# Kernel tuning notes

Measured on AMD Instinct MI355X. Metric: run time of the kernel, lower is better.

The kernel has to match this reference:

```python
import jax, jax.numpy as jnp
import numpy as np

B, N, DV = 32, 1024, 512
L, S, DT = 256, 8, 512
VOCAB = 1024
BAND = 16
LN_EPS = 1e-5


def setup_inputs() -> dict:
    key = jax.random.key(0)
    ks = jax.random.split(key, 12)
    w = lambda k, shp: jax.random.normal(k, shp, dtype=jnp.float32) * 0.02
    return {
        "vis_tokens": jax.random.normal(ks[0], (B, N, DV), dtype=jnp.float32),
        "txt_ctx_ids": jax.random.randint(ks[1], (B, L, S), 0, VOCAB, dtype=jnp.int32),
        "emb_w": w(ks[2], (VOCAB, DT)),        # embedding table, tied with classifier
        "wq": w(ks[3], (DV, DT)),              # q_proj: d_txt -> d_vis
        "wk": w(ks[4], (DV, DV)),
        "wv": w(ks[5], (DV, DV)),
        "wv2t": w(ks[6], (DT, DV)),            # vis2txt: d_vis -> d_txt
        "dw_k": w(ks[7], (DT, 1, 3)),          # depthwise conv1d kernel (O, I/g=1, K)
        "pw_k": w(ks[8], (DT, DT, 1)),         # pointwise conv1d kernel
        "ln_g": jnp.ones((DT,), jnp.float32),
        "ln_b": jnp.zeros((DT,), jnp.float32),
        "dir_alpha": jnp.float32(0.2),
    }


def reference(vis_tokens, txt_ctx_ids, emb_w, wq, wk, wv, wv2t, dw_k, pw_k, ln_g, ln_b, dir_alpha):
    b, n, dv = vis_tokens.shape
    E = emb_w[txt_ctx_ids]                       # [B, L, S, Dt]
    bl = b * E.shape[1]
    x = E.reshape(bl, E.shape[2], DT).transpose(0, 2, 1)  # [B*L, Dt, S]
    dn = ('NCH', 'OIH', 'NCH')
    h = jax.lax.conv_general_dilated(x, dw_k, (1,), 'SAME', dimension_numbers=dn,
                                     feature_group_count=DT)
    y = jax.lax.conv_general_dilated(jax.nn.silu(h), pw_k, (1,), 'SAME', dimension_numbers=dn)
    x = x + y
    m = x.mean(axis=2)                           # [B*L, Dt]
    mu = m.mean(-1, keepdims=True)
    var = ((m - mu) ** 2).mean(-1, keepdims=True)
    q_txt = ((m - mu) * jax.lax.rsqrt(var + LN_EPS) * ln_g + ln_b).reshape(b, -1, DT)  # [B, L, Dt]

    Q = q_txt @ wq.T                             # [B, L, Dv]
    K = vis_tokens @ wk.T                        # [B, N, Dv]
    V = vis_tokens @ wv.T
    logits = jnp.einsum('bld,bnd->bln', Q, K) * (dv ** -0.5)

    # linear centers (torch linspace(0, N-1, L).long() truncates toward zero)
    centers = jnp.linspace(0.0, n - 1, q_txt.shape[1]).astype(jnp.int32)  # [L]
    centers = jnp.broadcast_to(centers[None, :], (b, q_txt.shape[1]))
    idx = jnp.arange(n)[None, None, :]
    signed = (centers[..., None] - idx).astype(jnp.float32)
    logits = logits + dir_alpha * (signed / (BAND + 1e-6))
    keep = jnp.abs(idx - centers[..., None]) <= BAND
    logits = jnp.where(keep, logits, -jnp.inf)

    A = jax.nn.softmax(logits, axis=-1)          # [B, L, N]
    Fv = jnp.einsum('bln,bnd->bld', A, V)        # dropout in source is undefined attr; identity
    H = Fv @ wv2t.T                              # [B, L, Dt]
    cls = H @ emb_w.T                            # tied classifier
    return (cls, H, A)
```

## Files before the change

### kernel.cpp

```cpp
#include <hip/hip_runtime.h>
#include <cmath>

typedef unsigned short u16;
typedef __attribute__((ext_vector_type(8))) short bf16x8;
typedef __attribute__((ext_vector_type(4))) float f32x4;
typedef __attribute__((ext_vector_type(8))) unsigned short u16x8;

#define B_  32
#define N_  1024
#define L_  256
#define S_  8
#define DT_ 512
#define BAND_ 16

__device__ __forceinline__ u16 f2bf(float f) {
  union { float f; unsigned u; } x; x.f = f;
  unsigned r = (x.u + 0x7fffu + ((x.u >> 16) & 1u)) >> 16;
  return (u16)r;
}
__device__ __forceinline__ float bf2f(u16 h) {
  union { unsigned u; float f; } x; x.u = ((unsigned)h) << 16;
  return x.f;
}
__device__ __forceinline__ unsigned cvtpk(float lo, float hi) {
  unsigned r;
  asm volatile("v_cvt_pk_bf16_f32 %0, %1, %2" : "=v"(r) : "v"(lo), "v"(hi));
  return r;
}

#define B1_WAIT(N)                                       \
  asm volatile("s_waitcnt vmcnt(" #N ")" ::: "memory");  \
  __builtin_amdgcn_s_barrier();                          \
  __builtin_amdgcn_sched_barrier(0);
#define B2_BAR()                                         \
  __builtin_amdgcn_sched_barrier(0);                     \
  __builtin_amdgcn_s_barrier();

__global__ __launch_bounds__(256) void mega_front(
    const float* __restrict__ vis, u16* __restrict__ visb,
    const float* __restrict__ e, const float* __restrict__ q,
    const float* __restrict__ k, const float* __restrict__ v,
    const float* __restrict__ t, const float* __restrict__ pw,
    u16* __restrict__ eo, u16* __restrict__ qo, u16* __restrict__ kvo,
    u16* __restrict__ to, u16* __restrict__ po,
    const int* __restrict__ ids, const float* __restrict__ dwk,
    u16* __restrict__ shm, float* __restrict__ mbuf) {
  const int blk = blockIdx.x;
  const int tid = threadIdx.x;
  if (blk < 4096) {
    const int c0 = tid * 2;
#pragma unroll
    for (int ii = 0; ii < 2; ++ii) {
      const int bl = blk * 2 + ii;
      int sid[S_];
#pragma unroll
      for (int s = 0; s < S_; ++s) sid[s] = ids[bl * S_ + s];
      float2 x2[S_];
#pragma unroll
      for (int s = 0; s < S_; ++s)
        x2[s] = *(const float2*)(e + (size_t)sid[s] * DT_ + c0);
      const float2 d01 = *(const float2*)(dwk + 3 * c0 + 0);
      const float2 d23 = *(const float2*)(dwk + 3 * c0 + 2);
      const float2 d45 = *(const float2*)(dwk + 3 * c0 + 4);
      float me0 = 0.f, sh0 = 0.f, me1 = 0.f, sh1 = 0.f;
#pragma unroll
      for (int s = 0; s < S_; ++s) {
        const float xm0 = (s > 0) ? x2[s - 1].x : 0.0f;
        const float xp0 = (s < S_ - 1) ? x2[s + 1].x : 0.0f;
        const float xm1 = (s > 0) ? x2[s - 1].y : 0.0f;
        const float xp1 = (s < S_ - 1) ? x2[s + 1].y : 0.0f;
        const float h0 = d01.x * xm0 + d01.y * x2[s].x + d23.x * xp0;
        const float h1 = d23.y * xm1 + d45.x * x2[s].y + d45.y * xp1;
        sh0 += h0 / (1.0f + __expf(-h0));
        sh1 += h1 / (1.0f + __expf(-h1));
        me0 += x2[s].x;
        me1 += x2[s].y;
      }
      ((unsigned*)shm)[((size_t)bl * DT_ + c0) >> 1] =
          cvtpk(sh0 * (1.0f / S_), sh1 * (1.0f / S_));
      *(float2*)(mbuf + (size_t)bl * DT_ + c0) =
          make_float2(me0 * (1.0f / S_), me1 * (1.0f / S_));
    }
  } else {
    for (int ch = blk - 4096; ch < 18176; ch += 8192) {
      if (ch < 16384) {
        int i = ch * 256 + tid;
        float4 vv = ((const float4*)vis)[i];
        uint2 o;
        o.x = cvtpk(vv.x, vv.y);
        o.y = cvtpk(vv.z, vv.w);
        ((uint2*)visb)[i] = o;
      } else {
        int i = (ch - 16384) * 256 + tid;
        const float* src; u16* dst; int soff, doff;
        if (i < 131072)      { src = e;  dst = eo;  soff = i;          doff = soff; }
        else if (i < 196608) { src = q;  dst = qo;  soff = i - 131072; doff = soff; }
        else if (i < 262144) { src = k;  dst = kvo; soff = i - 196608; doff = soff; }
        else if (i < 327680) { src = v;  dst = kvo; soff = i - 262144; doff = soff + 65536; }
        else if (i < 393216) { src = t;  dst = to;  soff = i - 327680; doff = soff; }
        else                 { src = pw; dst = po;  soff = i - 393216; doff = soff; }
        float4 vv = ((const float4*)src)[soff];
        uint2 o;
        o.x = cvtpk(vv.x, vv.y);
        o.y = cvtpk(vv.z, vv.w);
        ((uint2*)dst)[doff] = o;
      }
    }
  }
}

__global__ __launch_bounds__(512) void gemm_kv_v2(
    const u16* __restrict__ A, const u16* __restrict__ B,
    u16* __restrict__ Cb, int M, int N, int K) {
  __shared__ u16 As[16384];
  __shared__ u16 Bs[8192];
  const int tid = threadIdx.x;
  const int w = tid >> 6;
  const int lane = tid & 63;
  const int wm = w >> 1, wn = w & 1;

  const int gx = gridDim.x;
  const int bid = blockIdx.y * gx + blockIdx.x;
  const int nwg = gx * gridDim.y;
  const int logical = (bid & 7) * (nwg >> 3) + (bid >> 3);
  const int bm = (logical / gx) << 8;
  const int bn = (logical % gx) << 7;

  const int rowA0 = (w << 5) + (lane >> 2);
  const int rowA1 = rowA0 + 16;
  const int rowB = (w << 4) + (lane >> 2);
  const int gac = (((lane & 3) ^ ((lane >> 3) & 3)) << 3);
  const u16* AgS0 = A + (size_t)(bm + rowA0) * K + gac;
  const u16* AgS1 = A + (size_t)(bm + rowA1) * K + gac;
  const u16* BgS = B + (size_t)(bn + rowB) * K + gac;
  const int ldsA0 = (w << 10);
  const int ldsA1 = (w << 10) + 512;
  const int ldsB = (w << 9);

#define STAGE(step)                                                           \
  {                                                                           \
    const int bufA_ = ((step) & 1) << 13;                                     \
    const int bufB_ = ((step) & 1) << 12;                                     \
    const int ks_ = (step) << 5;                                              \
    __builtin_amdgcn_global_load_lds(                                         \
        (const __attribute__((address_space(1))) void*)(AgS0 + ks_),          \
        (__attribute__((address_space(3))) void*)(As + bufA_ + ldsA0), 16, 0, 0); \
    __builtin_amdgcn_global_load_lds(                                         \
        (const __attribute__((address_space(1))) void*)(AgS1 + ks_),          \
        (__attribute__((address_space(3))) void*)(As + bufA_ + ldsA1), 16, 0, 0); \
    __builtin_amdgcn_global_load_lds(                                         \
        (const __attribute__((address_space(1))) void*)(BgS + ks_),           \
        (__attribute__((address_space(3))) void*)(Bs + bufB_ + ldsB), 16, 0, 0); \
  }

  const int kg = lane >> 4;
  int aoff[4], boff[4];
#pragma unroll
  for (int m = 0; m < 4; ++m) {
    const int r = (wm << 6) + (m << 4) + (lane & 15);
    aoff[m] = (r << 5) + ((kg ^ ((r >> 1) & 3)) << 3);
  }
#pragma unroll
  for (int n = 0; n < 4; ++n) {
    const int r = (wn << 6) + (n << 4) + (lane & 15);
    boff[n] = (r << 5) + ((kg ^ ((r >> 1) & 3)) << 3);
  }

  f32x4 acc[4][4];
#pragma unroll
  for (int m = 0; m < 4; ++m)
#pragma unroll
    for (int n = 0; n < 4; ++n) acc[m][n] = (f32x4){0.f, 0.f, 0.f, 0.f};

#define GROUP_BODY(sbuf)                                                      \
  {                                                                           \
    const u16* Ab = As + ((sbuf) << 13);                                      \
    const u16* Bb = Bs + ((sbuf) << 12);                                      \
    bf16x8 af[4], bfr[4];                                                     \
    _Pragma("unroll")                                                         \
    for (int m = 0; m < 4; ++m) af[m] = *(const bf16x8*)(Ab + aoff[m]);       \
    _Pragma("unroll")                                                         \
    for (int n = 0; n < 4; ++n) bfr[n] = *(const bf16x8*)(Bb + boff[n]);      \
    asm volatile("s_waitcnt lgkmcnt(0)" ::: "memory");                        \
    __builtin_amdgcn_sched_barrier(0);                                        \
    __builtin_amdgcn_s_setprio(1);                                            \
    _Pragma("unroll")                                                         \
    for (int m = 0; m < 4; ++m)                                               \
      _Pragma("unroll")                                                       \
      for (int n = 0; n < 4; ++n)                                             \
        acc[m][n] = __builtin_amdgcn_mfma_f32_16x16x32_bf16(                  \
            af[m], bfr[n], acc[m][n], 0, 0, 0);                               \
    __builtin_amdgcn_s_setprio(0);                                            \
  }

  const int nt = K >> 5;
  STAGE(0)
  for (int s = 0; s < nt; ++s) {
    __builtin_amdgcn_s_barrier();
    if (s + 1 < nt) {
      STAGE(s + 1)
      B1_WAIT(3)
    } else {
      B1_WAIT(0)
    }
    GROUP_BODY(s & 1)
  }
#undef GROUP_BODY
#undef STAGE

  const int rb = bm + (wm << 6) + ((lane >> 4) << 2);
  const int cb = bn + (wn << 6) + (lane & 15);
#pragma unroll
  for (int m = 0; m < 4; ++m)
#pragma unroll
    for (int n = 0; n < 4; ++n) {
      const int col = cb + (n << 4);
#pragma unroll
      for (int j = 0; j < 4; ++j) {
        size_t idx = (size_t)(rb + (m << 4) + j) * N + col;
        Cb[idx] = f2bf(acc[m][n][j]);
      }
    }
}

template <bool ACC, bool WF32, bool WBF16>
__global__ __launch_bounds__(256) void gemm_mfma(
    const u16* __restrict__ A, const u16* __restrict__ B,
    float* __restrict__ C, u16* __restrict__ Cb, int M, int N, int K) {
  __shared__ u16 As[8192];
  __shared__ u16 Bs[8192];
  const int tid = threadIdx.x;
  const int w = tid >> 6;
  const int lane = tid & 63;

  const int gx = gridDim.x;
  const int bid = blockIdx.y * gx + blockIdx.x;
  const int nwg = gx * gridDim.y;
  const int logical = (bid & 7) * (nwg >> 3) + (bid >> 3);
  const int bm = (logical / gx) << 7;
  const int bn = (logical % gx) << 7;
  const int wr = w >> 1, wc = w & 1;

  const int r0 = (w << 4) + (lane >> 2);
  const int kc = (lane & 3) << 3;
  const u16* Ag0 = A + (size_t)(bm + r0) * K + kc;
  const u16* Ag1 = Ag0 + (size_t)64 * K;
  const u16* Bg0 = B + (size_t)(bn + r0) * K + kc;
  const u16* Bg1 = Bg0 + (size_t)64 * K;

  int aoff[4], boff[4];
#pragma unroll
  for (int m = 0; m < 4; ++m)
    aoff[m] = (((wr << 6) + (m << 4) + (lane & 15)) << 5) + ((lane >> 4) << 3);
#pragma unroll
  for (int n = 0; n < 4; ++n)
    boff[n] = (((wc << 6) + (n << 4) + (lane & 15)) << 5) + ((lane >> 4) << 3);

  f32x4 acc[4][4];
#pragma unroll
  for (int m = 0; m < 4; ++m)
#pragma unroll
    for (int n = 0; n < 4; ++n) acc[m][n] = (f32x4){0.f, 0.f, 0.f, 0.f};

#define STAGE(buf, kt)                                                        \
  {                                                                           \
    u16* as_ = As + (buf) * 4096 + (w << 9);                                  \
    u16* bs_ = Bs + (buf) * 4096 + (w << 9);                                  \
    __builtin_amdgcn_global_load_lds(                                         \
        (const __attribute__((address_space(1))) void*)(Ag0 + (kt)),          \
        (__attribute__((address_space(3))) void*)as_, 16, 0, 0);              \
    __builtin_amdgcn_global_load_lds(                                         \
        (const __attribute__((address_space(1))) void*)(Ag1 + (kt)),          \
        (__attribute__((address_space(3))) void*)(as_ + 2048), 16, 0, 0);     \
    __builtin_amdgcn_global_load_lds(                                         \
        (const __attribute__((address_space(1))) void*)(Bg0 + (kt)),          \
        (__attribute__((address_space(3))) void*)bs_, 16, 0, 0);              \
    __builtin_amdgcn_global_load_lds(                                         \
        (const __attribute__((address_space(1))) void*)(Bg1 + (kt)),          \
        (__attribute__((address_space(3))) void*)(bs_ + 2048), 16, 0, 0);     \
  }

  const int nt = K >> 5;
  STAGE(0, 0);
  int cur = 0;
  for (int t = 0; t < nt; ++t) {
    if (t + 1 < nt) {
      STAGE(cur ^ 1, (t + 1) << 5);
      B1_WAIT(4)
    } else {
      B1_WAIT(0)
    }
    const u16* Ab = As + cur * 4096;
    const u16* Bb = Bs + cur * 4096;
    bf16x8 af[4], bfr[4];
#pragma unroll
    for (int m = 0; m < 4; ++m) af[m] = *(const bf16x8*)(Ab + aoff[m]);
#pragma unroll
    for (int n = 0; n < 4; ++n) bfr[n] = *(const bf16x8*)(Bb + boff[n]);
#pragma unroll
    for (int m = 0; m < 4; ++m)
#pragma unroll
      for (int n = 0; n < 4; ++n)
        acc[m][n] = __builtin_amdgcn_mfma_f32_16x16x32_bf16(
            af[m], bfr[n], acc[m][n], 0, 0, 0);
    B2_BAR()
    cur ^= 1;
  }
#undef STAGE

  const int rb = bm + (wr << 6) + ((lane >> 4) << 2);
  const int cb = bn + (wc << 6) + (lane & 15);
#pragma unroll
  for (int m = 0; m < 4; ++m)
#pragma unroll
    for (int n = 0; n < 4; ++n) {
      int col = cb + (n << 4);
#pragma unroll
      for (int j = 0; j < 4; ++j) {
        size_t idx = (size_t)(rb + (m << 4) + j) * N + col;
        float v = acc[m][n][j];
        if (ACC) v += C[idx];
        if (WF32) C[idx] = v;
        if (WBF16) Cb[idx] = f2bf(v);
      }
    }
}

template <bool ACC, bool WF32, bool WBF16>
__global__ __launch_bounds__(256) void gemm_n64(
    const u16* __restrict__ A, const u16* __restrict__ B,
    float* __restrict__ C, u16* __restrict__ Cb, int M, int N, int K) {
  __shared__ u16 As[8192];
  __shared__ u16 Bs[4096];
  const int tid = threadIdx.x;
  const int w = tid >> 6;
  const int lane = tid & 63;

  const int gx = gridDim.x;
  const int bid = blockIdx.y * gx + blockIdx.x;
  const int nwg = gx * gridDim.y;
  const int logical = (bid & 7) * (nwg >> 3) + (bid >> 3);
  const int bm = (logical / gx) << 7;
  const int bn = (logical % gx) << 6;

  const int r0 = (w << 4) + (lane >> 2);
  const int kc = (lane & 3) << 3;
  const u16* Ag0 = A + (size_t)(bm + r0) * K + kc;
  const u16* Ag1 = Ag0 + (size_t)64 * K;
  const u16* Bg0 = B + (size_t)(bn + r0) * K + kc;

  int aoff[2], boff[4];
#pragma unroll
  for (int m = 0; m < 2; ++m)
    aoff[m] = (((w << 5) + (m << 4) + (lane & 15)) << 5) + ((lane >> 4) << 3);
#pragma unroll
  for (int n = 0; n < 4; ++n)
    boff[n] = (((n << 4) + (lane & 15)) << 5) + ((lane >> 4) << 3);

  f32x4 acc[2][4];
#pragma unroll
  for (int m = 0; m < 2; ++m)
#pragma unroll
    for (int n = 0; n < 4; ++n) acc[m][n] = (f32x4){0.f, 0.f, 0.f, 0.f};

#define STAGE(buf, kt)                                                        \
  {                                                                           \
    u16* as_ = As + (buf) * 4096 + (w << 9);                                  \
    u16* bs_ = Bs + (buf) * 2048 + (w << 9);                                  \
    __builtin_amdgcn_global_load_lds(                                         \
        (const __attribute__((address_space(1))) void*)(Ag0 + (kt)),          \
        (__attribute__((address_space(3))) void*)as_, 16, 0, 0);              \
    __builtin_amdgcn_global_load_lds(                                         \
        (const __attribute__((address_space(1))) void*)(Ag1 + (kt)),          \
        (__attribute__((address_space(3))) void*)(as_ + 2048), 16, 0, 0);     \
    __builtin_amdgcn_global_load_lds(                                         \
        (const __attribute__((address_space(1))) void*)(Bg0 + (kt)),          \
        (__attribute__((address_space(3))) void*)bs_, 16, 0, 0);              \
  }

  const int nt = K >> 5;
  STAGE(0, 0);
  int cur = 0;
  for (int t = 0; t < nt; ++t) {
    if (t + 1 < nt) {
      STAGE(cur ^ 1, (t + 1) << 5);
      B1_WAIT(3)
    } else {
      B1_WAIT(0)
    }
    const u16* Ab = As + cur * 4096;
    const u16* Bb = Bs + cur * 2048;
    bf16x8 af[2], bfr[4];
#pragma unroll
    for (int m = 0; m < 2; ++m) af[m] = *(const bf16x8*)(Ab + aoff[m]);
#pragma unroll
    for (int n = 0; n < 4; ++n) bfr[n] = *(const bf16x8*)(Bb + boff[n]);
#pragma unroll
    for (int m = 0; m < 2; ++m)
#pragma unroll
      for (int n = 0; n < 4; ++n)
        acc[m][n] = __builtin_amdgcn_mfma_f32_16x16x32_bf16(
            af[m], bfr[n], acc[m][n], 0, 0, 0);
    B2_BAR()
    cur ^= 1;
  }
#undef STAGE

  const int rb = bm + (w << 5) + ((lane >> 4) << 2);
  const int cb = bn + (lane & 15);
#pragma unroll
  for (int m = 0; m < 2; ++m)
#pragma unroll
    for (int n = 0; n < 4; ++n) {
      int col = cb + (n << 4);
#pragma unroll
      for (int j = 0; j < 4; ++j) {
        size_t idx = (size_t)(rb + (m << 4) + j) * N + col;
        float v = acc[m][n][j];
        if (ACC) v += C[idx];
        if (WF32) C[idx] = v;
        if (WBF16) Cb[idx] = f2bf(v);
      }
    }
}

__global__ __launch_bounds__(256) void ln_kernel(
    const float* __restrict__ m, const float* __restrict__ g,
    const float* __restrict__ bta, u16* __restrict__ q) {
  int row = blockIdx.x;
  int tid = threadIdx.x;
  float v0 = m[(size_t)row * 512 + tid];
  float v1 = m[(size_t)row * 512 + 256 + tid];
  __shared__ float red[4], red2[4];
  float s = v0 + v1;
#pragma unroll
  for (int d = 32; d; d >>= 1) s += __shfl_xor(s, d);
  if ((tid & 63) == 0) red[tid >> 6] = s;
  __syncthreads();
  float mu = (red[0] + red[1] + red[2] + red[3]) * (1.0f / 512.0f);
  float d0 = v0 - mu, d1 = v1 - mu;
  float s2 = d0 * d0 + d1 * d1;
#pragma unroll
  for (int d = 32; d; d >>= 1) s2 += __shfl_xor(s2, d);
  if ((tid & 63) == 0) red2[tid >> 6] = s2;
  __syncthreads();
  float var = (red2[0] + red2[1] + red2[2] + red2[3]) * (1.0f / 512.0f);
  float r = rsqrtf(var + 1e-5f);
  q[(size_t)row * 512 + tid] = f2bf(d0 * r * g[tid] + bta[tid]);
  q[(size_t)row * 512 + 256 + tid] = f2bf(d1 * r * g[tid + 256] + bta[tid + 256]);
}

__global__ __launch_bounds__(512) void attn_kernel(
    const u16* __restrict__ Qb, const u16* __restrict__ KV,
    const float* __restrict__ alpha_p, float* __restrict__ A,
    u16* __restrict__ Fv) {
  __shared__ u16 KV_s[96 * 512];
  __shared__ u16 Q_s[16 * 520];
  __shared__ float S_s[16 * 100];

  const int bid = blockIdx.x;
  const int logical = (bid & 7) * 64 + (bid >> 3);
  const int b = logical >> 4, lg = logical & 15;
  const int l0 = lg * 16;
  const int tid = threadIdx.x;
  const int w = tid >> 6, lane = tid & 63;
  const float al = *alpha_p;

  const int c_min = (1023 * l0) / 255;
  const int kb0 = min(max(c_min - BAND_, 0), N_ - 96);

  {
    const size_t rowb = (size_t)(b * N_ + kb0);
    for (int rr = 0; rr < 12; ++rr) {
      const int r = w * 12 + rr;
      const u16* src = KV + (rowb + r) * 1024 + ((lane * 8) ^ ((r & 7) << 3));
      u16* dst = KV_s + r * 512;
      __builtin_amdgcn_global_load_lds(
          (const __attribute__((address_space(1))) void*)src,
          (__attribute__((address_space(3))) void*)dst, 16, 0, 0);
    }
  }
  {
    const int r = tid >> 5;
    const u16* qrow = Qb + (size_t)(b * L_ + l0 + r) * 512;
#pragma unroll
    for (int h = 0; h < 2; ++h) {
      const int ch = (tid & 31) + h * 32;
      u16x8 v = *(const u16x8*)(qrow + ch * 8);
      *(u16x8*)(Q_s + r * 520 + ch * 8) = v;
    }
  }
  __syncthreads();

  if (w < 6) {
    f32x4 acc = {0.f, 0.f, 0.f, 0.f};
    const int arow = (lane & 15) * 520 + ((lane >> 4) << 3);
    const int key = w * 16 + (lane & 15);
    const int swz = (key & 7) << 3;
    for (int ks = 0; ks < 16; ++ks) {
      bf16x8 aq = *(const bf16x8*)(Q_s + arow + ks * 32);
      bf16x8 bk =
          *(const bf16x8*)(KV_s + key * 512 + ((ks * 32 + ((lane >> 4) << 3)) ^ swz));
      acc = __builtin_amdgcn_mfma_f32_16x16x32_bf16(aq, bk, acc, 0, 0, 0);
    }
#pragma unroll
    for (int j = 0; j < 4; ++j)
      S_s[((lane >> 4) * 4 + j) * 100 + w * 16 + (lane & 15)] = acc[j];
  }
  __syncthreads();

  {
    const size_t rowb = (size_t)(b * N_ + kb0);
    for (int rr = 0; rr < 12; ++rr) {
      const int r = w * 12 + rr;
      const u16* src =
          KV + (rowb + r) * 1024 + 512 + ((lane * 8) ^ ((r & 7) << 3));
      u16* dst = KV_s + r * 512;
      __builtin_amdgcn_global_load_lds(
          (const __attribute__((address_space(1))) void*)src,
          (__attribute__((address_space(3))) void*)dst, 16, 0, 0);
    }
  }

#pragma unroll
  for (int rr = 0; rr < 2; ++rr) {
    const int l = 2 * w + rr;
    const int c = (1023 * (l0 + l)) / 255;
    const int g0 = kb0 + lane, g1 = kb0 + 64 + lane;
    const bool v0 = (g0 >= c - BAND_) && (g0 <= c + BAND_);
    const bool v1 = (lane < 32) && (g1 >= c - BAND_) && (g1 <= c + BAND_);
    const float sc = 0.044194173824159216f;
    float x0 = v0 ? S_s[l * 100 + lane] * sc +
                        al * ((float)(c - g0) * (1.0f / 16.000001f))
                  : -INFINITY;
    float x1 = v1 ? S_s[l * 100 + 64 + lane] * sc +
                        al * ((float)(c - g1) * (1.0f / 16.000001f))
                  : -INFINITY;
    float mx = fmaxf(x0, x1);
#pragma unroll
    for (int d = 32; d; d >>= 1) mx = fmaxf(mx, __shfl_xor(mx, d));
    float e0 = v0 ? expf(x0 - mx) : 0.0f;
    float e1 = v1 ? expf(x1 - mx) : 0.0f;
    float sm = e0 + e1;
#pragma unroll
    for (int d = 32; d; d >>= 1) sm += __shfl_xor(sm, d);
    const float inv = 1.0f / sm;
    S_s[l * 100 + lane] = e0 * inv;
    if (lane < 32) S_s[l * 100 + 64 + lane] = e1 * inv;
    const int lo = max(0, c - BAND_), hi = min(N_ - 1, c + BAND_);
    float* Arow = A + (size_t)(b * L_ + l0 + l) * N_;
#pragma unroll
    for (int p4 = 0; p4 < 4; ++p4) {
      const int p = (p4 * 64 + lane) * 4;
      float4 v;
      v.x = (p + 0 >= lo && p + 0 <= hi) ? S_s[l * 100 + p + 0 - kb0] : 0.0f;
      v.y = (p + 1 >= lo && p + 1 <= hi) ? S_s[l * 100 + p + 1 - kb0] : 0.0f;
      v.z = (p + 2 >= lo && p + 2 <= hi) ? S_s[l * 100 + p + 2 - kb0] : 0.0f;
      v.w = (p + 3 >= lo && p + 3 <= hi) ? S_s[l * 100 + p + 3 - kb0] : 0.0f;
      ((float4*)Arow)[p4 * 64 + lane] = v;
    }
  }
  __syncthreads();

#pragma unroll
  for (int rr = 0; rr < 2; ++rr) {
    const int l = 2 * w + rr;
    const int c = (1023 * (l0 + l)) / 255;
    const int jlo = max(0, c - BAND_) - kb0, jhi = min(N_ - 1, c + BAND_) - kb0;
    float acc[8] = {};
    for (int j = jlo; j <= jhi; ++j) {
      const float avj = S_s[l * 100 + j];
      const u16x8 v =
          *(const u16x8*)(KV_s + j * 512 + ((lane * 8) ^ ((j & 7) << 3)));
#pragma unroll
      for (int t = 0; t < 8; ++t) acc[t] += avj * bf2f(v[t]);
    }
    u16x8 fo;
#pragma unroll
    for (int t = 0; t < 8; ++t) fo[t] = f2bf(acc[t]);
    *(u16x8*)(Fv + (size_t)(b * L_ + l0 + l) * 512 + lane * 8) = fo;
  }
}

extern "C" void kernel_launch(void* const* d_in, const int* in_sizes, int n_in,
                              void* d_out, int out_size, void* d_ws,
                              size_t ws_size, hipStream_t stream) {
  const float* vis = (const float*)d_in[0];
  const int* ids = (const int*)d_in[1];
  const float* emb = (const float*)d_in[2];
  const float* wq = (const float*)d_in[3];
  const float* wk = (const float*)d_in[4];
  const float* wvp = (const float*)d_in[5];
  const float* wv2t = (const float*)d_in[6];
  const float* dwk = (const float*)d_in[7];
  const float* pwk = (const float*)d_in[8];
  const float* lng = (const float*)d_in[9];
  const float* lnb = (const float*)d_in[10];
  const float* alpha = (const float*)d_in[11];

  float* out_cls = (float*)d_out;
  float* out_H = out_cls + (size_t)8192 * 1024;
  float* out_A = out_H + (size_t)8192 * 512;

  char* p = (char*)d_ws;
  u16* visb = (u16*)p;              p += (size_t)32768 * 512 * 2;
  u16* KVb  = (u16*)p;              p += (size_t)32768 * 1024 * 2;
  u16* embb = (u16*)p;              p += (size_t)1024 * 512 * 2;
  u16* wqb  = (u16*)p;              p += (size_t)512 * 512 * 2;
  u16* wkvb = (u16*)p;              p += (size_t)1024 * 512 * 2;
  u16* wv2tb= (u16*)p;              p += (size_t)512 * 512 * 2;
  u16* pwkb = (u16*)p;              p += (size_t)512 * 512 * 2;
  u16* shmb = (u16*)p;              p += (size_t)8192 * 512 * 2;
  float* mbuf = (float*)p;          p += (size_t)8192 * 512 * 4;
  u16* qbuf = (u16*)p;              p += (size_t)8192 * 512 * 2;
  u16* Qbf  = (u16*)p;              p += (size_t)8192 * 512 * 2;
  u16* Fvb  = (u16*)p;              p += (size_t)8192 * 512 * 2;
  u16* Hb   = (u16*)p;              p += (size_t)8192 * 512 * 2;

  mega_front<<<12288, 256, 0, stream>>>(
      vis, visb, emb, wq, wk, wvp, wv2t, pwk,
      embb, wqb, wkvb, wv2tb, pwkb, ids, dwk, shmb, mbuf);

  gemm_kv_v2<<<dim3(8, 128), 512, 0, stream>>>(
      visb, wkvb, KVb, 32768, 1024, 512);

  gemm_n64<true, true, false><<<dim3(8, 64), 256, 0, stream>>>(
      shmb, pwkb, mbuf, nullptr, 8192, 512, 512);
  ln_kernel<<<8192, 256, 0, stream>>>(mbuf, lng, lnb, qbuf);
  gemm_n64<false, false, true><<<dim3(8, 64), 256, 0, stream>>>(
      qbuf, wqb, nullptr, Qbf, 8192, 512, 512);
  attn_kernel<<<512, 512, 0, stream>>>(Qbf, KVb, alpha, out_A, Fvb);
  gemm_n64<false, true, true><<<dim3(8, 64), 256, 0, stream>>>(
      Fvb, wv2tb, out_H, Hb, 8192, 512, 512);
  gemm_mfma<false, true, false><<<dim3(8, 64), 256, 0, stream>>>(
      Hb, embb, out_cls, nullptr, 8192, 1024, 512);
}
```

Baseline: 192.8 us.

## Triple-buffer KV GEMM LDS pipeline and restructure front conversion grid

The KV projection GEMM moves from double-buffered to triple-buffered LDS staging, prefetching two k-steps ahead so global-to-LDS loads have more time to land before they are consumed. In the front kernel, the grid-stride loop over conversion chunks is replaced by a larger grid where each thread converts two float4 elements, and the conv weight loads are hoisted out of the per-row loop. The SiLU division is replaced by a hardware reciprocal. The extra LDS buffer raises shared memory per block, which may reduce occupancy, and the reciprocal is slightly less precise than a true division.

```diff
diff --git a/kernel.cpp b/kernel.cpp
--- a/kernel.cpp
+++ b/kernel.cpp
@@ -49,6 +49,9 @@
   const int tid = threadIdx.x;
   if (blk < 4096) {
     const int c0 = tid * 2;
+    const float2 d01 = *(const float2*)(dwk + 3 * c0 + 0);
+    const float2 d23 = *(const float2*)(dwk + 3 * c0 + 2);
+    const float2 d45 = *(const float2*)(dwk + 3 * c0 + 4);
 #pragma unroll
     for (int ii = 0; ii < 2; ++ii) {
       const int bl = blk * 2 + ii;
@@ -59,9 +62,6 @@
 #pragma unroll
       for (int s = 0; s < S_; ++s)
         x2[s] = *(const float2*)(e + (size_t)sid[s] * DT_ + c0);
-      const float2 d01 = *(const float2*)(dwk + 3 * c0 + 0);
-      const float2 d23 = *(const float2*)(dwk + 3 * c0 + 2);
-      const float2 d45 = *(const float2*)(dwk + 3 * c0 + 4);
       float me0 = 0.f, sh0 = 0.f, me1 = 0.f, sh1 = 0.f;
 #pragma unroll
       for (int s = 0; s < S_; ++s) {
@@ -71,8 +71,8 @@
         const float xp1 = (s < S_ - 1) ? x2[s + 1].y : 0.0f;
         const float h0 = d01.x * xm0 + d01.y * x2[s].x + d23.x * xp0;
         const float h1 = d23.y * xm1 + d45.x * x2[s].y + d45.y * xp1;
-        sh0 += h0 / (1.0f + __expf(-h0));
-        sh1 += h1 / (1.0f + __expf(-h1));
+        sh0 += h0 * __builtin_amdgcn_rcpf(1.0f + __expf(-h0));
+        sh1 += h1 * __builtin_amdgcn_rcpf(1.0f + __expf(-h1));
         me0 += x2[s].x;
         me1 += x2[s].y;
       }
@@ -81,30 +81,32 @@
       *(float2*)(mbuf + (size_t)bl * DT_ + c0) =
           make_float2(me0 * (1.0f / S_), me1 * (1.0f / S_));
     }
+  } else if (blk < 12288) {
+    const int i0 = (blk - 4096) * 512 + tid;
+    const float4 v0 = ((const float4*)vis)[i0];
+    const float4 v1 = ((const float4*)vis)[i0 + 256];
+    uint2 o0, o1;
+    o0.x = cvtpk(v0.x, v0.y); o0.y = cvtpk(v0.z, v0.w);
+    o1.x = cvtpk(v1.x, v1.y); o1.y = cvtpk(v1.z, v1.w);
+    ((uint2*)visb)[i0] = o0;
+    ((uint2*)visb)[i0 + 256] = o1;
   } else {
-    for (int ch = blk - 4096; ch < 18176; ch += 8192) {
-      if (ch < 16384) {
-        int i = ch * 256 + tid;
-        float4 vv = ((const float4*)vis)[i];
-        uint2 o;
-        o.x = cvtpk(vv.x, vv.y);
-        o.y = cvtpk(vv.z, vv.w);
-        ((uint2*)visb)[i] = o;
-      } else {
-        int i = (ch - 16384) * 256 + tid;
-        const float* src; u16* dst; int soff, doff;
-        if (i < 131072)      { src = e;  dst = eo;  soff = i;          doff = soff; }
-        else if (i < 196608) { src = q;  dst = qo;  soff = i - 131072; doff = soff; }
-        else if (i < 262144) { src = k;  dst = kvo; soff = i - 196608; doff = soff; }
-        else if (i < 327680) { src = v;  dst = kvo; soff = i - 262144; doff = soff + 65536; }
-        else if (i < 393216) { src = t;  dst = to;  soff = i - 327680; doff = soff; }
-        else                 { src = pw; dst = po;  soff = i - 393216; doff = soff; }
-        float4 vv = ((const float4*)src)[soff];
-        uint2 o;
-        o.x = cvtpk(vv.x, vv.y);
-        o.y = cvtpk(vv.z, vv.w);
-        ((uint2*)dst)[doff] = o;
-      }
+    const int base = (blk - 12288) * 512 + tid;
+#pragma unroll
+    for (int jj = 0; jj < 2; ++jj) {
+      const int i = base + jj * 256;
+      const float* src; u16* dst; int soff, doff;
+      if (i < 131072)      { src = e;  dst = eo;  soff = i;          doff = soff; }
+      else if (i < 196608) { src = q;  dst = qo;  soff = i - 131072; doff = soff; }
+      else if (i < 262144) { src = k;  dst = kvo; soff = i - 196608; doff = soff; }
+      else if (i < 327680) { src = v;  dst = kvo; soff = i - 262144; doff = soff + 65536; }
+      else if (i < 393216) { src = t;  dst = to;  soff = i - 327680; doff = soff; }
+      else                 { src = pw; dst = po;  soff = i - 393216; doff = soff; }
+      float4 vv = ((const float4*)src)[soff];
+      uint2 o;
+      o.x = cvtpk(vv.x, vv.y);
+      o.y = cvtpk(vv.z, vv.w);
+      ((uint2*)dst)[doff] = o;
     }
   }
 }
@@ -112,8 +114,8 @@
 __global__ __launch_bounds__(512) void gemm_kv_v2(
     const u16* __restrict__ A, const u16* __restrict__ B,
     u16* __restrict__ Cb, int M, int N, int K) {
-  __shared__ u16 As[16384];
-  __shared__ u16 Bs[8192];
+  __shared__ u16 As[24576];
+  __shared__ u16 Bs[12288];
   const int tid = threadIdx.x;
   const int w = tid >> 6;
   const int lane = tid & 63;
@@ -139,8 +141,9 @@
 
 #define STAGE(step)                                                           \
   {                                                                           \
-    const int bufA_ = ((step) & 1) << 13;                                     \
-    const int bufB_ = ((step) & 1) << 12;                                     \
+    const int rb_ = (step) % 3;                                               \
+    const int bufA_ = rb_ * 8192;                                             \
+    const int bufB_ = rb_ * 4096;                                             \
     const int ks_ = (step) << 5;                                              \
     __builtin_amdgcn_global_load_lds(                                         \
         (const __attribute__((address_space(1))) void*)(AgS0 + ks_),          \
@@ -174,8 +177,8 @@
 
 #define GROUP_BODY(sbuf)                                                      \
   {                                                                           \
-    const u16* Ab = As + ((sbuf) << 13);                                      \
-    const u16* Bb = Bs + ((sbuf) << 12);                                      \
+    const u16* Ab = As + (sbuf) * 8192;                                       \
+    const u16* Bb = Bs + (sbuf) * 4096;                                       \
     bf16x8 af[4], bfr[4];                                                     \
     _Pragma("unroll")                                                         \
     for (int m = 0; m < 4; ++m) af[m] = *(const bf16x8*)(Ab + aoff[m]);       \
@@ -195,15 +198,18 @@
 
   const int nt = K >> 5;
   STAGE(0)
+  STAGE(1)
   for (int s = 0; s < nt; ++s) {
     __builtin_amdgcn_s_barrier();
-    if (s + 1 < nt) {
-      STAGE(s + 1)
+    if (s + 2 < nt) {
+      STAGE(s + 2)
+      B1_WAIT(6)
+    } else if (s + 1 < nt) {
       B1_WAIT(3)
     } else {
       B1_WAIT(0)
     }
-    GROUP_BODY(s & 1)
+    GROUP_BODY(s % 3)
   }
 #undef GROUP_BODY
 #undef STAGE
@@ -617,7 +623,7 @@
   u16* Fvb  = (u16*)p;              p += (size_t)8192 * 512 * 2;
   u16* Hb   = (u16*)p;              p += (size_t)8192 * 512 * 2;
 
-  mega_front<<<12288, 256, 0, stream>>>(
+  mega_front<<<13184, 256, 0, stream>>>(
       vis, visb, emb, wq, wk, wvp, wv2t, pwk,
       embb, wqb, wkvb, wv2tb, pwkb, ids, dwk, shmb, mbuf);
 
```

Result: faster. 188.3 us (-2.4%).
